# Kernel tuning notes

Hardware: AMD Instinct MI355X
Metric: run time of the kernel (lower is better)

## Reference

```python
import jax, jax.numpy as jnp
import numpy as np

B, S, D, H = 2, 2048, 1024, 16
HD = D // H  # head_dim = 64


def setup_inputs() -> dict:
    key = jax.random.key(0)
    k1, k2, k3, k4, k5 = jax.random.split(key, 5)
    x = jax.random.normal(k1, (B, S, D), dtype=jnp.float32)
    # causal additive mask [S, S]: 0 on/below diagonal, -1e9 above
    mask = jnp.where(jnp.tril(jnp.ones((S, S), dtype=bool)), 0.0, -1e9).astype(jnp.float32)
    scale = 1.0 / np.sqrt(D)
    W_qkv = jax.random.normal(k2, (D, 3 * D), dtype=jnp.float32) * scale
    b_qkv = jax.random.normal(k3, (3 * D,), dtype=jnp.float32) * 0.01
    W_o = jax.random.normal(k4, (D, D), dtype=jnp.float32) * scale
    b_o = jax.random.normal(k5, (D,), dtype=jnp.float32) * 0.01
    return {"x": x, "mask": mask, "W_qkv": W_qkv, "b_qkv": b_qkv, "W_o": W_o, "b_o": b_o}


def reference(x, mask, W_qkv, b_qkv, W_o, b_o):
    b, s, d = x.shape
    qkv = x @ W_qkv + b_qkv                         # [B,S,3D]
    qkv = qkv.reshape(b, s, H, 3 * HD).transpose(0, 2, 1, 3)  # [B,H,S,3*HD]
    q, k, v = jnp.split(qkv, 3, axis=-1)            # each [B,H,S,HD]
    scores = jnp.einsum('bhqd,bhkd->bhqk', q, k) / np.sqrt(HD)  # [B,H,S,S]
    scores = scores + mask                           # broadcast [S,S] additive mask
    attn = jax.nn.softmax(scores, axis=-1)
    vals = jnp.einsum('bhqk,bhkd->bhqd', attn, v)    # [B,H,S,HD]
    vals = vals.transpose(0, 2, 1, 3).reshape(b, s, d)
    return vals @ W_o + b_o
```

## Files before the change

kernel.cpp:

```cpp
#include <hip/hip_runtime.h>

#define NB 2
#define NS 2048
#define ND 1024
#define NH 16
#define NHD 64
#define QLD (3 * ND)
#define PADP 72
#define PADV 68

typedef unsigned short u16;
typedef __attribute__((ext_vector_type(8))) short short8;
typedef __attribute__((ext_vector_type(4))) short short4v;
typedef __attribute__((ext_vector_type(4))) float f32x4;

__device__ __forceinline__ u16 f2b(float f) {
    unsigned int x = __float_as_uint(f);
    return (u16)((x + 0x7fffu + ((x >> 16) & 1u)) >> 16);
}

__global__ __launch_bounds__(256) void convert_bf16(
    const float* __restrict__ src, u16* __restrict__ dst, int n)
{
    const int i = (blockIdx.x * 256 + threadIdx.x) * 8;
    if (i >= n) return;
    float4 a = *(const float4*)(src + i);
    float4 b = *(const float4*)(src + i + 4);
    *(ushort4*)(dst + i)     = make_ushort4(f2b(a.x), f2b(a.y), f2b(a.z), f2b(a.w));
    *(ushort4*)(dst + i + 4) = make_ushort4(f2b(b.x), f2b(b.y), f2b(b.z), f2b(b.w));
}

__global__ __launch_bounds__(256) void transpose_bf16(
    const float* __restrict__ W, u16* __restrict__ WT, int K, int N)
{
    __shared__ u16 Ts[64 * 72];
    const int t = threadIdx.x;
    const int k0 = blockIdx.y << 6, n0 = blockIdx.x << 6;
    const int r = t >> 4, c = (t & 15) << 2;
    #pragma unroll
    for (int rr = 0; rr < 64; rr += 16) {
        float4 v = *(const float4*)&W[(size_t)(k0 + r + rr) * N + n0 + c];
        Ts[(c + 0) * 72 + r + rr] = f2b(v.x);
        Ts[(c + 1) * 72 + r + rr] = f2b(v.y);
        Ts[(c + 2) * 72 + r + rr] = f2b(v.z);
        Ts[(c + 3) * 72 + r + rr] = f2b(v.w);
    }
    __syncthreads();
    const int n = t >> 2, cc = (t & 3) << 4;
    uint4 a = *(const uint4*)&Ts[n * 72 + cc];
    uint4 b = *(const uint4*)&Ts[n * 72 + cc + 8];
    *(uint4*)&WT[(size_t)(n0 + n) * K + k0 + cc]     = a;
    *(uint4*)&WT[(size_t)(n0 + n) * K + k0 + cc + 8] = b;
}

template <bool STORE_BF16>
__global__ __launch_bounds__(256) void gemm_mfma(
    const u16* __restrict__ A, const u16* __restrict__ BT,
    const float* __restrict__ bias,
    void* __restrict__ C, int M, int N, int K)
{
    __shared__ u16 As[128 * 32];
    __shared__ u16 Bs[128 * 32];

    const int tid = threadIdx.x;
    const int wave = tid >> 6, lane = tid & 63;
    const int col = lane & 15, quad = lane >> 4;
    const int wm = wave >> 1, wn = wave & 1;
    const int row0 = blockIdx.y << 7, col0 = blockIdx.x << 7;

    f32x4 acc[4][4] = {};

    const u16* asrc[2];
    const u16* bsrc[2];
    u16* adst[2];
    u16* bdst[2];
    #pragma unroll
    for (int is = 0; is < 2; ++is) {
        const int J = is * 256 + wave * 64 + lane;
        const int m = J >> 2;
        const int q = (J & 3) ^ ((m >> 1) & 3);
        asrc[is] = A  + (size_t)(row0 + m) * K + q * 8;
        bsrc[is] = BT + (size_t)(col0 + m) * K + q * 8;
        adst[is] = &As[(size_t)(is * 256 + wave * 64) * 8];
        bdst[is] = &Bs[(size_t)(is * 256 + wave * 64) * 8];
    }

    for (int kk = 0; kk < K; kk += 32) {
        __syncthreads();
        #pragma unroll
        for (int is = 0; is < 2; ++is) {
            __builtin_amdgcn_global_load_lds(
                (const __attribute__((address_space(1))) unsigned int*)(asrc[is] + kk),
                (__attribute__((address_space(3))) unsigned int*)adst[is], 16, 0, 0);
            __builtin_amdgcn_global_load_lds(
                (const __attribute__((address_space(1))) unsigned int*)(bsrc[is] + kk),
                (__attribute__((address_space(3))) unsigned int*)bdst[is], 16, 0, 0);
        }
        __syncthreads();

        short8 af[4], bf[4];
        #pragma unroll
        for (int i = 0; i < 4; ++i) {
            const int m = wm * 64 + i * 16 + col;
            af[i] = *(const short8*)&As[(m * 4 + (quad ^ ((m >> 1) & 3))) * 8];
        }
        #pragma unroll
        for (int j = 0; j < 4; ++j) {
            const int n = wn * 64 + j * 16 + col;
            bf[j] = *(const short8*)&Bs[(n * 4 + (quad ^ ((n >> 1) & 3))) * 8];
        }
        #pragma unroll
        for (int i = 0; i < 4; ++i)
            #pragma unroll
            for (int j = 0; j < 4; ++j)
                acc[i][j] = __builtin_amdgcn_mfma_f32_16x16x32_bf16(
                    af[i], bf[j], acc[i][j], 0, 0, 0);
    }

    #pragma unroll
    for (int j = 0; j < 4; ++j) {
        const int gc = col0 + wn * 64 + j * 16 + col;
        const float bj = bias[gc];
        #pragma unroll
        for (int i = 0; i < 4; ++i) {
            const int gr = row0 + wm * 64 + i * 16 + quad * 4;
            #pragma unroll
            for (int r = 0; r < 4; ++r) {
                const float v = acc[i][j][r] + bj;
                if (STORE_BF16)
                    ((u16*)C)[(size_t)(gr + r) * N + gc] = f2b(v);
                else
                    ((float*)C)[(size_t)(gr + r) * N + gc] = v;
            }
        }
    }
}

__global__ __launch_bounds__(256) void attn_kernel(
    const u16* __restrict__ qkv, u16* __restrict__ vals)
{
    __shared__ u16 Ks[2][64 * 64];
    __shared__ u16 Vt[2][64 * PADV];
    __shared__ u16 Ps[64 * PADP];

    const int tid = threadIdx.x;
    const int wave = tid >> 6, lane = tid & 63;
    const int col = lane & 15, quad = lane >> 4;
    const int qtA = blockIdx.x;
    const int qtB = 31 - qtA;
    const int bh = blockIdx.y;
    const int b = bh >> 4, h = bh & 15;
    const size_t base = (size_t)b * NS * QLD + (size_t)h * (3 * NHD);
    const int q0 = wave * 16;
    const int qloc = q0 + col;

    int Jrow[2], Jcol[2];
    #pragma unroll
    for (int is = 0; is < 2; ++is) {
        const int J = is * 256 + wave * 64 + lane;
        Jrow[is] = J >> 3;
        Jcol[is] = ((J & 7) ^ (Jrow[is] & 7)) << 3;
    }

    auto stage_tile = [&](int buf, int srow, int coloff) {
        #pragma unroll
        for (int is = 0; is < 2; ++is) {
            __builtin_amdgcn_global_load_lds(
                (const __attribute__((address_space(1))) unsigned int*)
                    (qkv + base + (size_t)(srow + Jrow[is]) * QLD + coloff + Jcol[is]),
                (__attribute__((address_space(3))) unsigned int*)
                    &Ks[buf][(size_t)(is * 256 + wave * 64) * 8], 16, 0, 0);
        }
    };
    auto read_frag = [&](int buf, int row, int half) -> short8 {
        const int blk = row * 8 + ((quad + (half << 2)) ^ (row & 7));
        return *(const short8*)&Ks[buf][blk << 3];
    };

    const int vtx = tid & 15, vty = tid >> 4;
    const int vk0 = vty << 2, vd0 = vtx << 2;
    auto load_vregs = [&](int kt, ushort4* vr) {
        const u16* vsrc = qkv + base + (size_t)(kt * 64 + vk0) * QLD + 2 * NHD + vd0;
        vr[0] = *(const ushort4*)(vsrc);
        vr[1] = *(const ushort4*)(vsrc + QLD);
        vr[2] = *(const ushort4*)(vsrc + 2 * QLD);
        vr[3] = *(const ushort4*)(vsrc + 3 * QLD);
    };
    auto write_vt = [&](int buf, const ushort4* vr) {
        *(ushort4*)&Vt[buf][(vd0 + 0) * PADV + vk0] =
            make_ushort4(vr[0].x, vr[1].x, vr[2].x, vr[3].x);
        *(ushort4*)&Vt[buf][(vd0 + 1) * PADV + vk0] =
            make_ushort4(vr[0].y, vr[1].y, vr[2].y, vr[3].y);
        *(ushort4*)&Vt[buf][(vd0 + 2) * PADV + vk0] =
            make_ushort4(vr[0].z, vr[1].z, vr[2].z, vr[3].z);
        *(ushort4*)&Vt[buf][(vd0 + 3) * PADV + vk0] =
            make_ushort4(vr[0].w, vr[1].w, vr[2].w, vr[3].w);
    };

    stage_tile(0, qtA * 64, 0);
    stage_tile(1, qtB * 64, 0);
    __syncthreads();
    short8 bqA0 = read_frag(0, qloc, 0), bqA1 = read_frag(0, qloc, 1);
    short8 bqB0 = read_frag(1, qloc, 0), bqB1 = read_frag(1, qloc, 1);
    __syncthreads();

    f32x4 accA[4] = {}, accB[4] = {};
    float mA = -1e30f, lA = 0.f, mB = -1e30f, lB = 0.f;

    auto process = [&](const short8& b0, const short8& b1,
                       short8 (*kb)[2], short8 (*vb)[2],
                       f32x4* accO, float& m, float& l, bool diag) {
        f32x4 s[4] = {};
        #pragma unroll
        for (int kg = 0; kg < 4; ++kg) {
            s[kg] = __builtin_amdgcn_mfma_f32_16x16x32_bf16(kb[kg][0], b0, s[kg], 0, 0, 0);
            s[kg] = __builtin_amdgcn_mfma_f32_16x16x32_bf16(kb[kg][1], b1, s[kg], 0, 0, 0);
        }
        #pragma unroll
        for (int kg = 0; kg < 4; ++kg)
            #pragma unroll
            for (int r = 0; r < 4; ++r) {
                float v = s[kg][r] * 0.125f;
                if (diag && (kg * 16 + quad * 4 + r > qloc)) v = -1e30f;
                s[kg][r] = v;
            }
        float mx = -1e30f;
        #pragma unroll
        for (int kg = 0; kg < 4; ++kg)
            mx = fmaxf(mx, fmaxf(fmaxf(s[kg][0], s[kg][1]), fmaxf(s[kg][2], s[kg][3])));
        mx = fmaxf(mx, __shfl_xor(mx, 16, 64));
        mx = fmaxf(mx, __shfl_xor(mx, 32, 64));
        const float mn = fmaxf(m, mx);
        const float alpha = __expf(m - mn);
        m = mn;

        float ps = 0.f;
        #pragma unroll
        for (int kg = 0; kg < 4; ++kg) {
            float p0 = __expf(s[kg][0] - mn);
            float p1 = __expf(s[kg][1] - mn);
            float p2 = __expf(s[kg][2] - mn);
            float p3 = __expf(s[kg][3] - mn);
            ps += (p0 + p1) + (p2 + p3);
            *(ushort4*)&Ps[qloc * PADP + kg * 16 + quad * 4] =
                make_ushort4(f2b(p0), f2b(p1), f2b(p2), f2b(p3));
        }
        ps += __shfl_xor(ps, 16, 64);
        ps += __shfl_xor(ps, 32, 64);
        l = l * alpha + ps;
        #pragma unroll
        for (int dg = 0; dg < 4; ++dg)
            #pragma unroll
            for (int r = 0; r < 4; ++r) accO[dg][r] *= alpha;

        short8 pb0 = *(const short8*)&Ps[qloc * PADP + quad * 8];
        short8 pb1 = *(const short8*)&Ps[qloc * PADP + 32 + quad * 8];
        #pragma unroll
        for (int dg = 0; dg < 4; ++dg) {
            accO[dg] = __builtin_amdgcn_mfma_f32_16x16x32_bf16(vb[dg][0], pb0, accO[dg], 0, 0, 0);
            accO[dg] = __builtin_amdgcn_mfma_f32_16x16x32_bf16(vb[dg][1], pb1, accO[dg], 0, 0, 0);
        }
    };

    ushort4 vcur[4], vnxt[4];
    stage_tile(0, 0, NHD);
    load_vregs(0, vcur);

    for (int kt = 0; kt <= qtB; ++kt) {
        const int cur = kt & 1, nxt = cur ^ 1;
        __syncthreads();
        write_vt(cur, vcur);
        __syncthreads();
        if (kt < qtB) {
            stage_tile(nxt, (kt + 1) * 64, NHD);
            load_vregs(kt + 1, vnxt);
        }

        short8 kb[4][2], vb[4][2];
        #pragma unroll
        for (int kg = 0; kg < 4; ++kg) {
            kb[kg][0] = read_frag(cur, kg * 16 + col, 0);
            kb[kg][1] = read_frag(cur, kg * 16 + col, 1);
        }
        #pragma unroll
        for (int dg = 0; dg < 4; ++dg) {
            const int n = dg * 16 + col;
            short4v lo0 = *(const short4v*)&Vt[cur][n * PADV + quad * 8];
            short4v hi0 = *(const short4v*)&Vt[cur][n * PADV + quad * 8 + 4];
            short4v lo1 = *(const short4v*)&Vt[cur][n * PADV + 32 + quad * 8];
            short4v hi1 = *(const short4v*)&Vt[cur][n * PADV + 32 + quad * 8 + 4];
            vb[dg][0] = __builtin_shufflevector(lo0, hi0, 0, 1, 2, 3, 4, 5, 6, 7);
            vb[dg][1] = __builtin_shufflevector(lo1, hi1, 0, 1, 2, 3, 4, 5, 6, 7);
        }

        process(bqB0, bqB1, kb, vb, accB, mB, lB, kt == qtB);
        if (kt <= qtA)
            process(bqA0, bqA1, kb, vb, accA, mA, lA, kt == qtA);

        #pragma unroll
        for (int i = 0; i < 4; ++i) vcur[i] = vnxt[i];
    }

    {
        const float inv = 1.f / lA;
        const size_t rowoff = ((size_t)b * NS + qtA * 64 + qloc) * ND + h * NHD;
        #pragma unroll
        for (int dg = 0; dg < 4; ++dg) {
            ushort4 o;
            o.x = f2b(accA[dg][0] * inv);
            o.y = f2b(accA[dg][1] * inv);
            o.z = f2b(accA[dg][2] * inv);
            o.w = f2b(accA[dg][3] * inv);
            *(ushort4*)(vals + rowoff + dg * 16 + quad * 4) = o;
        }
    }
    {
        const float inv = 1.f / lB;
        const size_t rowoff = ((size_t)b * NS + qtB * 64 + qloc) * ND + h * NHD;
        #pragma unroll
        for (int dg = 0; dg < 4; ++dg) {
            ushort4 o;
            o.x = f2b(accB[dg][0] * inv);
            o.y = f2b(accB[dg][1] * inv);
            o.z = f2b(accB[dg][2] * inv);
            o.w = f2b(accB[dg][3] * inv);
            *(ushort4*)(vals + rowoff + dg * 16 + quad * 4) = o;
        }
    }
}

extern "C" void kernel_launch(void* const* d_in, const int* in_sizes, int n_in,
                              void* d_out, int out_size, void* d_ws, size_t ws_size,
                              hipStream_t stream)
{
    const float* x    = (const float*)d_in[0];
    const float* Wqkv = (const float*)d_in[2];
    const float* bqkv = (const float*)d_in[3];
    const float* Wo   = (const float*)d_in[4];
    const float* bo   = (const float*)d_in[5];
    float* out = (float*)d_out;

    u16* x_bf   = (u16*)d_ws;
    u16* WqkvT  = x_bf   + (size_t)4096 * 1024;
    u16* WoT    = WqkvT  + (size_t)3072 * 1024;
    u16* qkv    = WoT    + (size_t)1024 * 1024;
    u16* vals   = qkv    + (size_t)4096 * 3072;

    const int M = NB * NS;

    convert_bf16<<<dim3(M * ND / (256 * 8)), dim3(256), 0, stream>>>(
        x, x_bf, M * ND);
    transpose_bf16<<<dim3(QLD / 64, ND / 64), dim3(256), 0, stream>>>(
        Wqkv, WqkvT, ND, QLD);
    transpose_bf16<<<dim3(ND / 64, ND / 64), dim3(256), 0, stream>>>(
        Wo, WoT, ND, ND);

    gemm_mfma<true><<<dim3(QLD / 128, M / 128), dim3(256), 0, stream>>>(
        x_bf, WqkvT, bqkv, qkv, M, QLD, ND);
    attn_kernel<<<dim3(16, NB * NH), dim3(256), 0, stream>>>(qkv, vals);
    gemm_mfma<false><<<dim3(ND / 128, M / 128), dim3(256), 0, stream>>>(
        vals, WoT, bo, out, M, ND, ND);
}
```

Before: 221.0 us.

## Interleave dual-tile attention stages, lazy rescale, packed bf16 cvt, narrower out-proj tiles

The attention loop now splits the per-tile work into QK, softmax and PV phases and interleaves the two query tiles, with a separate P buffer for each, so MFMA work from one tile can overlap softmax of the other. MFMA sections are bracketed with s_setprio. The online softmax skips rescaling when the new max exceeds the old by no more than 8, and bf16 packing uses v_cvt_pk_bf16_f32. The output-projection GEMM is templated on BN and launched with 64-wide column tiles, doubling its block count for better CU occupancy. The lazy-rescale threshold allows unnormalized exponentials up to e^8, which may cost some numeric headroom.

```diff
diff --git a/kernel.cpp b/kernel.cpp
--- a/kernel.cpp
+++ b/kernel.cpp
@@ -19,6 +19,12 @@
     return (u16)((x + 0x7fffu + ((x >> 16) & 1u)) >> 16);
 }
 
+__device__ __forceinline__ unsigned int cvtpk(float lo, float hi) {
+    unsigned int r;
+    asm("v_cvt_pk_bf16_f32 %0, %1, %2" : "=v"(r) : "v"(lo), "v"(hi));
+    return r;
+}
+
 __global__ __launch_bounds__(256) void convert_bf16(
     const float* __restrict__ src, u16* __restrict__ dst, int n)
 {
@@ -53,73 +59,82 @@
     *(uint4*)&WT[(size_t)(n0 + n) * K + k0 + cc + 8] = b;
 }
 
-template <bool STORE_BF16>
+template <int BN, bool STORE_BF16>
 __global__ __launch_bounds__(256) void gemm_mfma(
     const u16* __restrict__ A, const u16* __restrict__ BT,
     const float* __restrict__ bias,
     void* __restrict__ C, int M, int N, int K)
 {
+    constexpr int BIS = BN / 64;
+    constexpr int NJ  = BN / 32;
     __shared__ u16 As[128 * 32];
-    __shared__ u16 Bs[128 * 32];
+    __shared__ u16 Bs[BN * 32];
 
     const int tid = threadIdx.x;
     const int wave = tid >> 6, lane = tid & 63;
     const int col = lane & 15, quad = lane >> 4;
     const int wm = wave >> 1, wn = wave & 1;
-    const int row0 = blockIdx.y << 7, col0 = blockIdx.x << 7;
-
-    f32x4 acc[4][4] = {};
+    const int row0 = blockIdx.y << 7, col0 = blockIdx.x * BN;
+
+    f32x4 acc[4][NJ] = {};
 
     const u16* asrc[2];
-    const u16* bsrc[2];
     u16* adst[2];
-    u16* bdst[2];
     #pragma unroll
     for (int is = 0; is < 2; ++is) {
         const int J = is * 256 + wave * 64 + lane;
         const int m = J >> 2;
         const int q = (J & 3) ^ ((m >> 1) & 3);
-        asrc[is] = A  + (size_t)(row0 + m) * K + q * 8;
+        asrc[is] = A + (size_t)(row0 + m) * K + q * 8;
+        adst[is] = &As[(size_t)(is * 256 + wave * 64) * 8];
+    }
+    const u16* bsrc[BIS];
+    u16* bdst[BIS];
+    #pragma unroll
+    for (int is = 0; is < BIS; ++is) {
+        const int J = is * 256 + wave * 64 + lane;
+        const int m = J >> 2;
+        const int q = (J & 3) ^ ((m >> 1) & 3);
         bsrc[is] = BT + (size_t)(col0 + m) * K + q * 8;
-        adst[is] = &As[(size_t)(is * 256 + wave * 64) * 8];
         bdst[is] = &Bs[(size_t)(is * 256 + wave * 64) * 8];
     }
 
     for (int kk = 0; kk < K; kk += 32) {
         __syncthreads();
         #pragma unroll
-        for (int is = 0; is < 2; ++is) {
+        for (int is = 0; is < 2; ++is)
             __builtin_amdgcn_global_load_lds(
                 (const __attribute__((address_space(1))) unsigned int*)(asrc[is] + kk),
                 (__attribute__((address_space(3))) unsigned int*)adst[is], 16, 0, 0);
+        #pragma unroll
+        for (int is = 0; is < BIS; ++is)
             __builtin_amdgcn_global_load_lds(
                 (const __attribute__((address_space(1))) unsigned int*)(bsrc[is] + kk),
                 (__attribute__((address_space(3))) unsigned int*)bdst[is], 16, 0, 0);
-        }
         __syncthreads();
 
-        short8 af[4], bf[4];
+        short8 af[4], bf[NJ];
         #pragma unroll
         for (int i = 0; i < 4; ++i) {
             const int m = wm * 64 + i * 16 + col;
             af[i] = *(const short8*)&As[(m * 4 + (quad ^ ((m >> 1) & 3))) * 8];
         }
         #pragma unroll
-        for (int j = 0; j < 4; ++j) {
-            const int n = wn * 64 + j * 16 + col;
+        for (int j = 0; j < NJ; ++j) {
+            const int n = wn * (BN / 2) + j * 16 + col;
             bf[j] = *(const short8*)&Bs[(n * 4 + (quad ^ ((n >> 1) & 3))) * 8];
         }
         #pragma unroll
         for (int i = 0; i < 4; ++i)
             #pragma unroll
-            for (int j = 0; j < 4; ++j)
+            for (int j = 0; j < NJ; ++j)
                 acc[i][j] = __builtin_amdgcn_mfma_f32_16x16x32_bf16(
                     af[i], bf[j], acc[i][j], 0, 0, 0);
     }
 
     #pragma unroll
-    for (int j = 0; j < 4; ++j) {
-        const int gc = col0 + wn * 64 + j * 16 + col;
+    for (int j = 0; j < NJ; ++j) {
+        const int gc = col0 + wn * (BN / 2) + j * 16 + col;
         const float bj = bias[gc];
         #pragma unroll
         for (int i = 0; i < 4; ++i) {
@@ -141,7 +156,7 @@
 {
     __shared__ u16 Ks[2][64 * 64];
     __shared__ u16 Vt[2][64 * PADV];
-    __shared__ u16 Ps[64 * PADP];
+    __shared__ u16 Ps[2][64 * PADP];
 
     const int tid = threadIdx.x;
     const int wave = tid >> 6, lane = tid & 63;
@@ -207,15 +222,19 @@
     f32x4 accA[4] = {}, accB[4] = {};
     float mA = -1e30f, lA = 0.f, mB = -1e30f, lB = 0.f;
 
-    auto process = [&](const short8& b0, const short8& b1,
-                       short8 (*kb)[2], short8 (*vb)[2],
-                       f32x4* accO, float& m, float& l, bool diag) {
-        f32x4 s[4] = {};
+    auto qk = [&](const short8& b0, const short8& b1,
+                  short8 (&kb)[4][2], f32x4 (&s)[4]) {
+        __builtin_amdgcn_s_setprio(1);
         #pragma unroll
         for (int kg = 0; kg < 4; ++kg) {
             s[kg] = __builtin_amdgcn_mfma_f32_16x16x32_bf16(kb[kg][0], b0, s[kg], 0, 0, 0);
             s[kg] = __builtin_amdgcn_mfma_f32_16x16x32_bf16(kb[kg][1], b1, s[kg], 0, 0, 0);
         }
+        __builtin_amdgcn_s_setprio(0);
+    };
+
+    auto sm = [&](f32x4 (&s)[4], f32x4 (&accO)[4], float& m, float& l,
+                  bool diag, u16* ps) {
         #pragma unroll
         for (int kg = 0; kg < 4; ++kg)
             #pragma unroll
@@ -230,36 +249,44 @@
             mx = fmaxf(mx, fmaxf(fmaxf(s[kg][0], s[kg][1]), fmaxf(s[kg][2], s[kg][3])));
         mx = fmaxf(mx, __shfl_xor(mx, 16, 64));
         mx = fmaxf(mx, __shfl_xor(mx, 32, 64));
-        const float mn = fmaxf(m, mx);
-        const float alpha = __expf(m - mn);
-        m = mn;
-
-        float ps = 0.f;
+        if (!__all(mx <= m + 8.f)) {
+            const float mn = fmaxf(m, mx);
+            const float alpha = __expf(m - mn);
+            m = mn;
+            l *= alpha;
+            #pragma unroll
+            for (int dg = 0; dg < 4; ++dg)
+                #pragma unroll
+                for (int r = 0; r < 4; ++r) accO[dg][r] *= alpha;
+        }
+        float psum = 0.f;
         #pragma unroll
         for (int kg = 0; kg < 4; ++kg) {
-            float p0 = __expf(s[kg][0] - mn);
-            float p1 = __expf(s[kg][1] - mn);
-            float p2 = __expf(s[kg][2] - mn);
-            float p3 = __expf(s[kg][3] - mn);
-            ps += (p0 + p1) + (p2 + p3);
-            *(ushort4*)&Ps[qloc * PADP + kg * 16 + quad * 4] =
-                make_ushort4(f2b(p0), f2b(p1), f2b(p2), f2b(p3));
-        }
-        ps += __shfl_xor(ps, 16, 64);
-        ps += __shfl_xor(ps, 32, 64);
-        l = l * alpha + ps;
-        #pragma unroll
-        for (int dg = 0; dg < 4; ++dg)
-            #pragma unroll
-            for (int r = 0; r < 4; ++r) accO[dg][r] *= alpha;
-
-        short8 pb0 = *(const short8*)&Ps[qloc * PADP + quad * 8];
-        short8 pb1 = *(const short8*)&Ps[qloc * PADP + 32 + quad * 8];
+            float p0 = __expf(s[kg][0] - m);
+            float p1 = __expf(s[kg][1] - m);
+            float p2 = __expf(s[kg][2] - m);
+            float p3 = __expf(s[kg][3] - m);
+            psum += (p0 + p1) + (p2 + p3);
+            uint2 w;
+            w.x = cvtpk(p0, p1);
+            w.y = cvtpk(p2, p3);
+            *(uint2*)&ps[qloc * PADP + kg * 16 + quad * 4] = w;
+        }
+        psum += __shfl_xor(psum, 16, 64);
+        psum += __shfl_xor(psum, 32, 64);
+        l += psum;
+    };
+
+    auto pv = [&](short8 (&vb)[4][2], f32x4 (&accO)[4], const u16* ps) {
+        short8 pb0 = *(const short8*)&ps[qloc * PADP + quad * 8];
+        short8 pb1 = *(const short8*)&ps[qloc * PADP + 32 + quad * 8];
+        __builtin_amdgcn_s_setprio(1);
         #pragma unroll
         for (int dg = 0; dg < 4; ++dg) {
             accO[dg] = __builtin_amdgcn_mfma_f32_16x16x32_bf16(vb[dg][0], pb0, accO[dg], 0, 0, 0);
             accO[dg] = __builtin_amdgcn_mfma_f32_16x16x32_bf16(vb[dg][1], pb1, accO[dg], 0, 0, 0);
         }
+        __builtin_amdgcn_s_setprio(0);
     };
 
     ushort4 vcur[4], vnxt[4];
@@ -293,9 +320,20 @@
             vb[dg][1] = __builtin_shufflevector(lo1, hi1, 0, 1, 2, 3, 4, 5, 6, 7);
         }
 
-        process(bqB0, bqB1, kb, vb, accB, mB, lB, kt == qtB);
-        if (kt <= qtA)
-            process(bqA0, bqA1, kb, vb, accA, mA, lA, kt == qtA);
+        if (kt <= qtA) {
+            f32x4 sB[4] = {}, sA[4] = {};
+            qk(bqB0, bqB1, kb, sB);
+            qk(bqA0, bqA1, kb, sA);
+            sm(sB, accB, mB, lB, false, Ps[0]);
+            sm(sA, accA, mA, lA, kt == qtA, Ps[1]);
+            pv(vb, accB, Ps[0]);
+            pv(vb, accA, Ps[1]);
+        } else {
+            f32x4 sB[4] = {};
+            qk(bqB0, bqB1, kb, sB);
+            sm(sB, accB, mB, lB, kt == qtB, Ps[0]);
+            pv(vb, accB, Ps[0]);
+        }
 
         #pragma unroll
         for (int i = 0; i < 4; ++i) vcur[i] = vnxt[i];
@@ -306,12 +344,10 @@
         const size_t rowoff = ((size_t)b * NS + qtA * 64 + qloc) * ND + h * NHD;
         #pragma unroll
         for (int dg = 0; dg < 4; ++dg) {
-            ushort4 o;
-            o.x = f2b(accA[dg][0] * inv);
-            o.y = f2b(accA[dg][1] * inv);
-            o.z = f2b(accA[dg][2] * inv);
-            o.w = f2b(accA[dg][3] * inv);
-            *(ushort4*)(vals + rowoff + dg * 16 + quad * 4) = o;
+            uint2 o;
+            o.x = cvtpk(accA[dg][0] * inv, accA[dg][1] * inv);
+            o.y = cvtpk(accA[dg][2] * inv, accA[dg][3] * inv);
+            *(uint2*)(vals + rowoff + dg * 16 + quad * 4) = o;
         }
     }
     {
@@ -319,12 +355,10 @@
         const size_t rowoff = ((size_t)b * NS + qtB * 64 + qloc) * ND + h * NHD;
         #pragma unroll
         for (int dg = 0; dg < 4; ++dg) {
-            ushort4 o;
-            o.x = f2b(accB[dg][0] * inv);
-            o.y = f2b(accB[dg][1] * inv);
-            o.z = f2b(accB[dg][2] * inv);
-            o.w = f2b(accB[dg][3] * inv);
-            *(ushort4*)(vals + rowoff + dg * 16 + quad * 4) = o;
+            uint2 o;
+            o.x = cvtpk(accB[dg][0] * inv, accB[dg][1] * inv);
+            o.y = cvtpk(accB[dg][2] * inv, accB[dg][3] * inv);
+            *(uint2*)(vals + rowoff + dg * 16 + quad * 4) = o;
         }
     }
 }
@@ -355,9 +389,9 @@
     transpose_bf16<<<dim3(ND / 64, ND / 64), dim3(256), 0, stream>>>(
         Wo, WoT, ND, ND);
 
-    gemm_mfma<true><<<dim3(QLD / 128, M / 128), dim3(256), 0, stream>>>(
+    gemm_mfma<128, true><<<dim3(QLD / 128, M / 128), dim3(256), 0, stream>>>(
         x_bf, WqkvT, bqkv, qkv, M, QLD, ND);
     attn_kernel<<<dim3(16, NB * NH), dim3(256), 0, stream>>>(qkv, vals);
-    gemm_mfma<false><<<dim3(ND / 128, M / 128), dim3(256), 0, stream>>>(
+    gemm_mfma<64, false><<<dim3(ND / 64, M / 128), dim3(256), 0, stream>>>(
         vals, WoT, bo, out, M, ND, ND);
 }
```

After: 220.0 us. About the same (-0.5%).
